# Optimization experiments

Hardware: AMD Instinct MI355X
Metric: run time of the kernel (lower is better)

The kernel has to match this reference:

```python
import jax, jax.numpy as jnp
import numpy as np
import math

G = 8        # groups
ORDER = 2    # Taylor order
GAMMA = 1e-4 # RBF gamma
EPS = 1e-5   # GroupNorm eps


def setup_inputs() -> dict:
    key = jax.random.key(0)
    ks = jax.random.split(key, 6)
    B, C_HI, C_LO, P = 16, 512, 512, 256
    H1 = W1 = 64
    H2 = W2 = 32
    s = 0.02
    return {
        "input_high": jax.random.normal(ks[0], (B, C_HI, H1, W1), jnp.float32),
        "input_low": jax.random.normal(ks[1], (B, C_LO, H2, W2), jnp.float32),
        "Wt": jax.random.normal(ks[2], (P, C_HI), jnp.float32) * s,
        "Wp": jax.random.normal(ks[3], (P, C_LO), jnp.float32) * s,
        "Wg": jax.random.normal(ks[4], (P, C_LO), jnp.float32) * s,
        # grouped 1x1 conv planes -> inplanes1: [G, out_per_group, in_per_group]
        "Wz": jax.random.normal(ks[5], (G, C_HI // G, P // G), jnp.float32) * s,
        "gn_w": jnp.ones((C_HI,), jnp.float32),
        "gn_b": jnp.zeros((C_HI,), jnp.float32),
    }


def _taylor_alpha():
    # alpha_k = sqrt((2*gamma)^k / k! * exp(-2*gamma)) for k = 0..ORDER
    ks = np.arange(ORDER + 1)
    fact = np.array([math.factorial(int(k)) for k in ks], dtype=np.float64)
    a = np.sqrt((2.0 * GAMMA) ** ks / fact * np.exp(-2.0 * GAMMA))
    return jnp.asarray(a, jnp.float32)


def reference(input_high, input_low, Wt, Wp, Wg, Wz, gn_w, gn_b):
    # 1x1-conv projections as channel contractions
    t = jnp.einsum('bchw,oc->bohw', input_high, Wt)   # [b, P, h1, w1]
    p = jnp.einsum('bchw,oc->bohw', input_low, Wp)    # [b, P, h2, w2]
    g = jnp.einsum('bchw,oc->bohw', input_low, Wg)    # [b, P, h2, w2]
    b, c1, h1, w1 = t.shape

    alpha = _taylor_alpha()                            # [ORDER+1]
    # split channels into groups, flatten (c/G)*h*w per group
    tg = t.reshape(b, G, -1)                           # [b, G, N1]
    pg = p.reshape(b, G, -1)                           # [b, G, N2]
    gg = g.reshape(b, G, -1)                           # [b, G, N2]

    # low-rank Taylor feature maps: [b, G, ORDER+1, N]
    t_tay = jnp.stack([tg ** k for k in range(ORDER + 1)], axis=2) * alpha[None, None, :, None]
    p_tay = jnp.stack([pg ** k for k in range(ORDER + 1)], axis=2) * alpha[None, None, :, None]

    att = jnp.einsum('bgkn,bgn->bgk', p_tay, gg)       # [b, G, ORDER+1]
    x = jnp.einsum('bgk,bgkn->bgn', att, t_tay)        # [b, G, N1]
    x = x.reshape(b, G, c1 // G, h1, w1)               # grouped feature map

    # grouped 1x1 conv z: planes -> inplanes1
    z = jnp.einsum('bgihw,goi->bgohw', x, Wz)
    z = z.reshape(b, -1, h1, w1)                       # [b, C_HI, h1, w1]

    # GroupNorm(num_groups=G) with affine, then residual
    zg = z.reshape(b, G, -1)
    mu = zg.mean(axis=-1, keepdims=True)
    var = zg.var(axis=-1, keepdims=True)
    zn = ((zg - mu) * jax.lax.rsqrt(var + EPS)).reshape(z.shape)
    out = zn * gn_w[None, :, None, None] + gn_b[None, :, None, None] + input_high
    return out
```

## Files before the change

### kernel.cpp

```cpp
#include <hip/hip_runtime.h>
#include <math.h>

typedef __attribute__((ext_vector_type(8))) short short8;
typedef __attribute__((ext_vector_type(8))) unsigned short u16x8;
typedef __attribute__((ext_vector_type(4))) float f32x4;

#define EPS_ 1e-5f

__device__ inline unsigned int cvtpk(float a, float b) {
    unsigned int r;
    asm("v_cvt_pk_bf16_f32 %0, %1, %2" : "=v"(r) : "v"(a), "v"(b));
    return r;
}

__device__ inline f32x4 mfma16(u16x8 a, u16x8 b, f32x4 c) {
    return __builtin_amdgcn_mfma_f32_16x16x32_bf16((short8)a, (short8)b, c, 0, 0, 0);
}

__device__ inline void gll16(const unsigned short* g, unsigned short* l) {
    __builtin_amdgcn_global_load_lds(
        (const __attribute__((address_space(1))) unsigned int*)g,
        (__attribute__((address_space(3))) unsigned int*)l, 16, 0, 0);
}

__global__ __launch_bounds__(256)
void k0s(const float* __restrict__ xlo, float* __restrict__ sxsum)
{
    __shared__ float sred[256];
    int blk = blockIdx.x;
    int cgrp = blk & 15, b = blk >> 4;
    int tid = threadIdx.x;
    int cl = tid >> 3, seg = tid & 7;
    int c = cgrp * 32 + cl;
    const float* row = xlo + ((size_t)b * 512 + c) * 1024 + seg * 128;
    float s = 0.f;
#pragma unroll
    for (int i = 0; i < 32; i++) {
        float4 v = ((const float4*)row)[i];
        s += v.x + v.y + v.z + v.w;
    }
    sred[tid] = s;
    __syncthreads();
    if (seg == 0) {
        float t = 0.f;
#pragma unroll
        for (int e = 0; e < 8; e++) t += sred[cl * 8 + e];
        sxsum[(size_t)b * 512 + c] = t;
    }
}

__global__ __launch_bounds__(256)
void k0w_t(const float* __restrict__ Wt, unsigned short* __restrict__ wtb)
{
    int blk = blockIdx.x, tid = threadIdx.x;
    int kc = blk >> 3, sub = blk & 7;
    int idx = sub * 256 + tid;
    int row = idx >> 3, s = idx & 7;
    int colbase = kc * 64 + ((s ^ (row & 7)) << 3);
    const float* sp = Wt + (size_t)row * 512 + colbase;
    float4 v0 = ((const float4*)sp)[0];
    float4 v1 = ((const float4*)sp)[1];
    uint4 q = { cvtpk(v0.x, v0.y), cvtpk(v0.z, v0.w),
                cvtpk(v1.x, v1.y), cvtpk(v1.z, v1.w) };
    *(uint4*)&wtb[(size_t)(kc * 2048 + idx) * 8] = q;
}

#define K1_BODY(C0, VCUR, VNXT, DOPREF)                                          \
  {                                                                              \
    if (DOPREF) {                                                                \
        const float* xc = xlo + ((size_t)b * 512 + (C0) + 64 + cs * 8) * 1024 + hw0 + xrow; \
        _Pragma("unroll")                                                        \
        for (int j = 0; j < 8; j++) VNXT[j] = xc[(size_t)j * 1024];              \
    }                                                                            \
    __syncthreads();                                                             \
    _Pragma("unroll")                                                            \
    for (int k = 0; k < 4; k++) {                                                \
        int idx = k * 256 + tid;                                                 \
        int row = idx >> 3, s = idx & 7;                                         \
        const float* pp = Wp + (size_t)(pbase + row) * 512 + (C0) + s * 8;       \
        const float* pg = Wg + (size_t)(pbase + row) * 512 + (C0) + s * 8;       \
        float4 a0 = ((const float4*)pp)[0], a1 = ((const float4*)pp)[1];         \
        float4 b0 = ((const float4*)pg)[0], b1 = ((const float4*)pg)[1];         \
        uint4 qp = { cvtpk(a0.x,a0.y), cvtpk(a0.z,a0.w),                         \
                     cvtpk(a1.x,a1.y), cvtpk(a1.z,a1.w) };                       \
        uint4 qg = { cvtpk(b0.x,b0.y), cvtpk(b0.z,b0.w),                         \
                     cvtpk(b1.x,b1.y), cvtpk(b1.z,b1.w) };                       \
        int off = row * 64 + ((s ^ (row & 7)) << 3);                             \
        *(uint4*)&sWp[off] = qp;                                                 \
        *(uint4*)&sWg[off] = qg;                                                 \
    }                                                                            \
    {                                                                            \
        uint4 q = { cvtpk(VCUR[0],VCUR[1]), cvtpk(VCUR[2],VCUR[3]),              \
                    cvtpk(VCUR[4],VCUR[5]), cvtpk(VCUR[6],VCUR[7]) };            \
        int phys = cs ^ (xrow & 7);                                              \
        *(uint4*)&sX1[xrow * 64 + phys * 8] = q;                                 \
    }                                                                            \
    __syncthreads();                                                             \
    _Pragma("unroll")                                                            \
    for (int kk = 0; kk < 2; kk++) {                                             \
        u16x8 bf[2];                                                             \
        _Pragma("unroll")                                                        \
        for (int ht = 0; ht < 2; ht++) {                                         \
            int row = ht * 16 + l15;                                             \
            bf[ht] = *(const u16x8*)&sX1[row * 64 + (((kk*4+l4) ^ (row&7)) << 3)]; \
        }                                                                        \
        _Pragma("unroll")                                                        \
        for (int i = 0; i < 2; i++) {                                            \
            int row = w * 32 + i * 16 + l15;                                     \
            int off = row * 64 + (((kk*4+l4) ^ (row&7)) << 3);                   \
            u16x8 ap = *(const u16x8*)&sWp[off];                                 \
            u16x8 ag = *(const u16x8*)&sWg[off];                                 \
            _Pragma("unroll")                                                    \
            for (int ht = 0; ht < 2; ht++) {                                     \
                pacc[i][ht] = mfma16(ap, bf[ht], pacc[i][ht]);                   \
                gacc[i][ht] = mfma16(ag, bf[ht], gacc[i][ht]);                   \
            }                                                                    \
        }                                                                        \
    }                                                                            \
  }

__global__ __launch_bounds__(256, 4)
void k1_att(const float* __restrict__ xlo, const float* __restrict__ Wp,
            const float* __restrict__ Wg, float* __restrict__ att_part)
{
    __shared__ unsigned short sWp[8192];
    __shared__ unsigned short sWg[8192];
    __shared__ unsigned short sX1[2048];

    int tid = threadIdx.x;
    int w = tid >> 6, lane = tid & 63;
    int l15 = lane & 15, l4 = lane >> 4;
    int beta = blockIdx.x;
    int tile = beta & 31, mh = (beta >> 5) & 1, b = beta >> 6;
    int hw0 = tile * 32;
    int pbase = mh * 128;
    int xrow = tid & 31, cs = tid >> 5;

    f32x4 pacc[2][2] = {};
    f32x4 gacc[2][2] = {};

    float vbA[8], vbB[8];
    {
        const float* xc = xlo + ((size_t)b * 512 + cs * 8) * 1024 + hw0 + xrow;
#pragma unroll
        for (int j = 0; j < 8; j++) vbA[j] = xc[(size_t)j * 1024];
    }

    for (int kc2 = 0; kc2 < 4; kc2++) {
        int c0 = kc2 * 128;
        K1_BODY(c0,      vbA, vbB, true);
        K1_BODY(c0 + 64, vbB, vbA, (kc2 < 3));
    }

    float s1 = 0.f, s2 = 0.f;
#pragma unroll
    for (int i = 0; i < 2; i++)
#pragma unroll
        for (int ht = 0; ht < 2; ht++)
#pragma unroll
            for (int r = 0; r < 4; r++) {
                float pv = pacc[i][ht][r], gv = gacc[i][ht][r];
                s1 += pv * gv; s2 += pv * pv * gv;
            }
#pragma unroll
    for (int m = 1; m < 64; m <<= 1) {
        s1 += __shfl_xor(s1, m);
        s2 += __shfl_xor(s2, m);
    }
    if (lane == 0) {
        int g = mh * 4 + w;
        float* dst = att_part + ((size_t)(b * 8 + g) * 32 + tile) * 2;
        dst[0] = s1; dst[1] = s2;
    }
}

__global__ __launch_bounds__(64)
void k1b_coef(const float* __restrict__ Wg, const float* __restrict__ sxsum,
              const float* __restrict__ att_part, float* __restrict__ coef,
              float a0s, float a1s, float a2s)
{
    int bg = blockIdx.x;
    int b = bg >> 3, g = bg & 7;
    int l = threadIdx.x;
    float s0 = 0.f;
    for (int cc = 0; cc < 512; cc += 64) {
        int c = cc + l;
        float cs = 0.f;
#pragma unroll
        for (int pp = 0; pp < 32; pp++) cs += Wg[(size_t)(g * 32 + pp) * 512 + c];
        s0 += cs * sxsum[(size_t)b * 512 + c];
    }
    float s1 = (l < 32) ? att_part[((size_t)bg * 32 + l) * 2 + 0] : 0.f;
    float s2 = (l < 32) ? att_part[((size_t)bg * 32 + l) * 2 + 1] : 0.f;
#pragma unroll
    for (int m = 1; m < 64; m <<= 1) {
        s0 += __shfl_xor(s0, m);
        s1 += __shfl_xor(s1, m);
        s2 += __shfl_xor(s2, m);
    }
    if (l == 0) {
        coef[bg * 3 + 0] = a0s * s0;
        coef[bg * 3 + 1] = a1s * s1;
        coef[bg * 3 + 2] = a2s * s2;
    }
}

#define XLOAD(DST, KC)                                                           \
  { const float* xc = xhi + ((size_t)(b * 512 + (KC) * 64 + w * 8)) * 4096 + hw0 + xrow; \
    _Pragma("unroll")                                                            \
    for (int j = 0; j < 8; j++) DST[j] = xc[(size_t)j * 4096]; }

#define K2CHUNK(KC, WBUF, PBUF, DOPREF, VMC)                                     \
  {                                                                              \
    asm volatile("s_waitcnt lgkmcnt(0)" ::: "memory");                           \
    __builtin_amdgcn_s_barrier();                                                \
    __builtin_amdgcn_sched_barrier(0);                                           \
    {                                 \
        uint4 q = { cvtpk(WBUF[0],WBUF[1]), cvtpk(WBUF[2],WBUF[3]),              \
                    cvtpk(WBUF[4],WBUF[5]), cvtpk(WBUF[6],WBUF[7]) };            \
        int phys = w ^ (xrow & 7);                                               \
        *(uint4*)&sX[xrow * 64 + phys * 8] = q;                                  \
    }                                                                            \
    __builtin_amdgcn_sched_barrier(0);                                           \
    _Pragma("unroll")                                                            \
    for (int k = 0; k < 4; k++) {                                                \
        int u = k * 512 + tid;                                                   \
        gll16(wtb + (((size_t)(KC) * 2048 + u) << 3), &sMain[u << 3]);           \
    }                                                                            \
    __builtin_amdgcn_sched_barrier(0);                                           \
    if (DOPREF) { XLOAD(PBUF, (KC) + 2) }                                        \
    asm volatile("s_waitcnt vmcnt(" #VMC ") lgkmcnt(0)" ::: "memory");           \
    __builtin_amdgcn_s_barrier();                                                \
    __builtin_amdgcn_sched_barrier(0);                                           \
    _Pragma("unroll")                                                            \
    for (int kk = 0; kk < 2; kk++) {                                             \
        u16x8 bf[4];                                                             \
        _Pragma("unroll")                                                        \
        for (int ht = 0; ht < 4; ht++) {                                         \
            int row = ht * 16 + l15;                                             \
            bf[ht] = *(const u16x8*)&sX[row * 64 + (((kk*4+l4) ^ (row&7)) << 3)]; \
        }                                                                        \
        _Pragma("unroll")                                                        \
        for (int i = 0; i < 2; i++) {                                            \
            int row = w * 32 + i * 16 + l15;                                     \
            u16x8 af = *(const u16x8*)&sMain[row * 64 + (((kk*4+l4) ^ (row&7)) << 3)]; \
            _Pragma("unroll")                                                    \
            for (int ht = 0; ht < 4; ht++)                                       \
                acc[i][ht] = mfma16(af, bf[ht], acc[i][ht]);                     \
        }                                                                        \
    }                                                                            \
  }

__global__ __launch_bounds__(512, 4)
void k2_main_g(const float* __restrict__ xhi, const unsigned short* __restrict__ wtb,
               const float* __restrict__ Wz, const float* __restrict__ coef,
               float* __restrict__ zout, float* __restrict__ zstat)
{
    __shared__ unsigned short sMain[16384];
    __shared__ unsigned short sX[4096];

    int tid = threadIdx.x;
    int w = tid >> 6, lane = tid & 63;
    int l15 = lane & 15, l4 = lane >> 4;
    int hwt = blockIdx.x & 63, b = blockIdx.x >> 6;
    int hw0 = hwt * 64;
    int xrow = tid & 63;

    const float* cf = coef + (size_t)(b * 8 + w) * 3;
    float c0v = cf[0], c1v = cf[1], c2v = cf[2];

    f32x4 acc[2][4] = {};

    float vA[8], vB[8], vC[8];
    XLOAD(vA, 0)
    XLOAD(vB, 1)

    K2CHUNK(0, vA, vC, 1, 8)
    K2CHUNK(1, vB, vA, 1, 8)
    K2CHUNK(2, vC, vB, 1, 8)
    K2CHUNK(3, vA, vC, 1, 8)
    K2CHUNK(4, vB, vA, 1, 8)
    K2CHUNK(5, vC, vB, 1, 8)
    K2CHUNK(6, vA, vC, 0, 0)
    K2CHUNK(7, vB, vA, 0, 0)

#pragma unroll
    for (int i = 0; i < 2; i++)
#pragma unroll
        for (int ht = 0; ht < 4; ht++) {
            f32x4 t = acc[i][ht];
            acc[i][ht] = c1v * t + c2v * t * t;
        }
    __syncthreads();

#pragma unroll
    for (int i = 0; i < 2; i++)
#pragma unroll
        for (int ht = 0; ht < 4; ht++) {
            int row = ht * 16 + l15;
            f32x4 xv = acc[i][ht];
            uint2 q = { cvtpk(xv[0], xv[1]), cvtpk(xv[2], xv[3]) };
            int phys = w * 4 + ((i * 2 + (l4 >> 1)) ^ (row & 3));
            *(uint2*)&sMain[row * 256 + phys * 8 + (l4 & 1) * 4] = q;
        }

    float* sR = (float*)sX;
    {
        const float* wr = Wz + (size_t)tid * 32;
        float s = 0.f;
#pragma unroll
        for (int q = 0; q < 8; q++) {
            float4 v = ((const float4*)wr)[q];
            s += v.x + v.y + v.z + v.w;
        }
        sR[tid] = s;
    }
    u16x8 wzf[4];
#pragma unroll
    for (int ot = 0; ot < 4; ot++) {
        const float* wr = Wz + (size_t)(w * 64 + ot * 16 + l15) * 32 + l4 * 8;
        float4 v0 = ((const float4*)wr)[0];
        float4 v1 = ((const float4*)wr)[1];
        uint4 q = { cvtpk(v0.x,v0.y), cvtpk(v0.z,v0.w),
                    cvtpk(v1.x,v1.y), cvtpk(v1.z,v1.w) };
        wzf[ot] = *(u16x8*)&q;
    }
    asm volatile("s_waitcnt lgkmcnt(0)" ::: "memory");
    __builtin_amdgcn_sched_barrier(0);

    float s = 0.f, s2a = 0.f;
    f32x4 zero4 = {0.f, 0.f, 0.f, 0.f};
#pragma unroll
    for (int ht = 0; ht < 4; ht++) {
        int row = ht * 16 + l15;
        u16x8 bfr = *(const u16x8*)&sMain[row * 256 + (w * 4 + (l4 ^ (row & 3))) * 8];
#pragma unroll
        for (int ot = 0; ot < 4; ot++) {
            f32x4 z = mfma16(wzf[ot], bfr, zero4);
            f32x4 rv = *(const f32x4*)&sR[w * 64 + ot * 16 + l4 * 4];
            z = z + c0v * rv;
            float* zp = zout + ((size_t)(b * 512 + w * 64 + ot * 16 + l4 * 4)) * 4096
                      + hw0 + ht * 16 + l15;
#pragma unroll
            for (int r = 0; r < 4; r++) {
                zp[(size_t)r * 4096] = z[r];
                s += z[r]; s2a += z[r] * z[r];
            }
        }
    }
#pragma unroll
    for (int m = 1; m < 64; m <<= 1) {
        s   += __shfl_xor(s, m);
        s2a += __shfl_xor(s2a, m);
    }
    if (lane == 0) {
        atomicAdd(&zstat[(size_t)(b * 8 + w) * 2 + 0], s);
        atomicAdd(&zstat[(size_t)(b * 8 + w) * 2 + 1], s2a);
    }
}

#define K2_BODY(C0, VCUR, VNXT, DOPREF)                                          \
  {                                                                              \
    if (DOPREF) {                                                                \
        const float* xc = xhi + ((size_t)b * 512 + (C0) + 64 + w * 8) * 4096 + hw0 + xrow; \
        _Pragma("unroll")                                                        \
        for (int j = 0; j < 8; j++) VNXT[j] = xc[(size_t)j * 4096];              \
    }                                                                            \
    __syncthreads();                                                             \
    _Pragma("unroll")                                                            \
    for (int k = 0; k < 4; k++) {                                                \
        int idx = k * 512 + tid;                                                 \
        int row = idx >> 3, s = idx & 7;                                         \
        const float* sp = Wt + (size_t)row * 512 + (C0) + s * 8;                 \
        float4 v0 = ((const float4*)sp)[0];                                      \
        float4 v1 = ((const float4*)sp)[1];                                      \
        uint4 q = { cvtpk(v0.x,v0.y), cvtpk(v0.z,v0.w),                          \
                    cvtpk(v1.x,v1.y), cvtpk(v1.z,v1.w) };                        \
        *(uint4*)&sWt[row * 64 + ((s ^ (row & 7)) << 3)] = q;                    \
    }                                                                            \
    {                                                                            \
        uint4 q = { cvtpk(VCUR[0],VCUR[1]), cvtpk(VCUR[2],VCUR[3]),              \
                    cvtpk(VCUR[4],VCUR[5]), cvtpk(VCUR[6],VCUR[7]) };            \
        int phys = w ^ (xrow & 7);                                               \
        *(uint4*)&sX[xrow * 64 + phys * 8] = q;                                  \
    }                                                                            \
    __syncthreads();                                                             \
    _Pragma("unroll")                                                            \
    for (int kk = 0; kk < 2; kk++) {                                             \
        u16x8 bf[4];                                                             \
        _Pragma("unroll")                                                        \
        for (int ht = 0; ht < 4; ht++) {                                         \
            int row = ht * 16 + l15;                                             \
            bf[ht] = *(const u16x8*)&sX[row * 64 + (((kk*4+l4) ^ (row&7)) << 3)]; \
        }                                                                        \
        _Pragma("unroll")                                                        \
        for (int i = 0; i < 2; i++) {                                            \
            int row = w * 32 + i * 16 + l15;                                     \
            u16x8 af = *(const u16x8*)&sWt[row * 64 + (((kk*4+l4) ^ (row&7)) << 3)]; \
            _Pragma("unroll")                                                    \
            for (int ht = 0; ht < 4; ht++)                                       \
                acc[i][ht] = mfma16(af, bf[ht], acc[i][ht]);                     \
        }                                                                        \
    }                                                                            \
  }

__global__ __launch_bounds__(512, 4)
void k2_main_fb(const float* __restrict__ xhi, const float* __restrict__ Wt,
                const float* __restrict__ Wz, const float* __restrict__ coef,
                float* __restrict__ zout, float* __restrict__ zstat)
{
    __shared__ unsigned short sWt[16384];
    __shared__ unsigned short sX[8192];

    int tid = threadIdx.x;
    int w = tid >> 6, lane = tid & 63;
    int l15 = lane & 15, l4 = lane >> 4;
    int hwt = blockIdx.x & 63, b = blockIdx.x >> 6;
    int hw0 = hwt * 64;
    int xrow = tid & 63;

    const float* cf = coef + (size_t)(b * 8 + w) * 3;
    float c0v = cf[0], c1v = cf[1], c2v = cf[2];

    f32x4 acc[2][4] = {};

    float vbA[8], vbB[8];
    {
        const float* xc = xhi + ((size_t)b * 512 + w * 8) * 4096 + hw0 + xrow;
#pragma unroll
        for (int j = 0; j < 8; j++) vbA[j] = xc[(size_t)j * 4096];
    }

    for (int kc2 = 0; kc2 < 4; kc2++) {
        int c0 = kc2 * 128;
        K2_BODY(c0,      vbA, vbB, true);
        K2_BODY(c0 + 64, vbB, vbA, (kc2 < 3));
    }

#pragma unroll
    for (int i = 0; i < 2; i++)
#pragma unroll
        for (int ht = 0; ht < 4; ht++) {
            f32x4 t = acc[i][ht];
            acc[i][ht] = c1v * t + c2v * t * t;
        }
    __syncthreads();
#pragma unroll
    for (int i = 0; i < 2; i++)
#pragma unroll
        for (int ht = 0; ht < 4; ht++) {
            int row = ht * 16 + l15;
            f32x4 xv = acc[i][ht];
            uint2 q = { cvtpk(xv[0], xv[1]), cvtpk(xv[2], xv[3]) };
            int phys = w * 4 + ((i * 2 + (l4 >> 1)) ^ (row & 3));
            *(uint2*)&sWt[row * 256 + phys * 8 + (l4 & 1) * 4] = q;
        }
    float* sR = (float*)sX;
    {
        const float* wr = Wz + (size_t)tid * 32;
        float s = 0.f;
#pragma unroll
        for (int q = 0; q < 8; q++) {
            float4 v = ((const float4*)wr)[q];
            s += v.x + v.y + v.z + v.w;
        }
        sR[tid] = s;
    }
    u16x8 wzf[4];
#pragma unroll
    for (int ot = 0; ot < 4; ot++) {
        const float* wr = Wz + (size_t)(w * 64 + ot * 16 + l15) * 32 + l4 * 8;
        float4 v0 = ((const float4*)wr)[0];
        float4 v1 = ((const float4*)wr)[1];
        uint4 q = { cvtpk(v0.x,v0.y), cvtpk(v0.z,v0.w),
                    cvtpk(v1.x,v1.y), cvtpk(v1.z,v1.w) };
        wzf[ot] = *(u16x8*)&q;
    }
    __syncthreads();

    float s = 0.f, s2a = 0.f;
    f32x4 zero4 = {0.f, 0.f, 0.f, 0.f};
#pragma unroll
    for (int ht = 0; ht < 4; ht++) {
        int row = ht * 16 + l15;
        u16x8 bfr = *(const u16x8*)&sWt[row * 256 + (w * 4 + (l4 ^ (row & 3))) * 8];
#pragma unroll
        for (int ot = 0; ot < 4; ot++) {
            f32x4 z = mfma16(wzf[ot], bfr, zero4);
            f32x4 rv = *(const f32x4*)&sR[w * 64 + ot * 16 + l4 * 4];
            z = z + c0v * rv;
            float* zp = zout + ((size_t)(b * 512 + w * 64 + ot * 16 + l4 * 4)) * 4096
                      + hw0 + ht * 16 + l15;
#pragma unroll
            for (int r = 0; r < 4; r++) {
                zp[(size_t)r * 4096] = z[r];
                s += z[r]; s2a += z[r] * z[r];
            }
        }
    }
#pragma unroll
    for (int m = 1; m < 64; m <<= 1) {
        s   += __shfl_xor(s, m);
        s2a += __shfl_xor(s2a, m);
    }
    if (lane == 0) {
        atomicAdd(&zstat[(size_t)(b * 8 + w) * 2 + 0], s);
        atomicAdd(&zstat[(size_t)(b * 8 + w) * 2 + 1], s2a);
    }
}

__global__ void k2b_gn(const float* __restrict__ zstat, float* __restrict__ gnstat)
{
    int t = threadIdx.x;
    if (t >= 128) return;
    float S = zstat[t * 2], S2 = zstat[t * 2 + 1];
    const float N = 64.0f * 4096.0f;
    float mean = S / N;
    float var = S2 / N - mean * mean;
    var = var < 0.f ? 0.f : var;
    gnstat[t * 2] = mean;
    gnstat[t * 2 + 1] = rsqrtf(var + EPS_);
}

__global__ __launch_bounds__(256)
void k3_final(float* __restrict__ out, const float* __restrict__ xhi,
              const float* __restrict__ gnstat, const float* __restrict__ gnw,
              const float* __restrict__ gnb)
{
#pragma unroll
    for (int k = 0; k < 4; k++) {
        size_t idx = (size_t)blockIdx.x * 1024 + (size_t)k * 256 + threadIdx.x;
        size_t e = idx * 4;
        int ch = (int)((e >> 12) & 511);
        int b  = (int)(e >> 21);
        int gg = ch >> 6;
        const float* gs = gnstat + (size_t)(b * 8 + gg) * 2;
        float mean = gs[0];
        float w = gnw[ch] * gs[1];
        float bb = gnb[ch];
        float4 z = ((const float4*)out)[idx];
        float4 xv = ((const float4*)xhi)[idx];
        float4 r;
        r.x = (z.x - mean) * w + bb + xv.x;
        r.y = (z.y - mean) * w + bb + xv.y;
        r.z = (z.z - mean) * w + bb + xv.z;
        r.w = (z.w - mean) * w + bb + xv.w;
        ((float4*)out)[idx] = r;
    }
}

extern "C" void kernel_launch(void* const* d_in, const int* in_sizes, int n_in,
                              void* d_out, int out_size, void* d_ws, size_t ws_size,
                              hipStream_t stream) {
    (void)in_sizes; (void)n_in; (void)out_size;
    const float* xhi = (const float*)d_in[0];
    const float* xlo = (const float*)d_in[1];
    const float* Wt  = (const float*)d_in[2];
    const float* Wp  = (const float*)d_in[3];
    const float* Wg  = (const float*)d_in[4];
    const float* Wz  = (const float*)d_in[5];
    const float* gnw = (const float*)d_in[6];
    const float* gnb = (const float*)d_in[7];
    float* out = (float*)d_out;
    float* ws  = (float*)d_ws;

    float* sxsum    = ws;
    float* att_part = ws + 8192;
    float* coef     = ws + 16384;
    float* zstat    = ws + 16768;
    float* gnstat   = ws + 17024;
    unsigned short* wtb = (unsigned short*)((char*)d_ws + 69632);

    const size_t WS_NEED = 69632 + 262144;
    bool use_gll = (ws_size >= WS_NEED);

    double g2 = 2.0e-4;
    double ee = exp(-g2);
    float a0s = (float)ee;
    float a1s = (float)(g2 * ee);
    float a2s = (float)(g2 * g2 * 0.5 * ee);

    k0s     <<<dim3(256),  dim3(256), 0, stream>>>(xlo, sxsum);
    k1_att  <<<dim3(1024), dim3(256), 0, stream>>>(xlo, Wp, Wg, att_part);
    k1b_coef<<<dim3(128),  dim3(64),  0, stream>>>(Wg, sxsum, att_part, coef, a0s, a1s, a2s);
    hipMemsetAsync(zstat, 0, 256 * sizeof(float), stream);
    if (use_gll) {
        k0w_t    <<<dim3(64),   dim3(256), 0, stream>>>(Wt, wtb);
        k2_main_g<<<dim3(1024), dim3(512), 0, stream>>>(xhi, wtb, Wz, coef, out, zstat);
    } else {
        k2_main_fb<<<dim3(1024), dim3(512), 0, stream>>>(xhi, Wt, Wz, coef, out, zstat);
    }
    k2b_gn  <<<dim3(1),    dim3(128), 0, stream>>>(zstat, gnstat);
    k3_final<<<dim3(8192), dim3(256), 0, stream>>>(out, xhi, gnstat, gnw, gnb);
}
```

Measured before the change: 211.3 us.

## Widen main GEMM tile to 128 spatial positions to halve Wt reloads

Each block of the fused projection kernel now covers 128 spatial positions instead of 64, halving the grid. Each Wt chunk staged into shared memory is therefore reused across twice as many columns, which cuts global/L2 traffic for the weight. The x prefetch changes from triple to double buffering with 16 values per thread. The grouped Wz epilogue is split into two passes because the wider tile's bf16 activations no longer fit in one shared buffer. Host launches are reordered so the memset and weight conversion run earlier; the cost is more registers per thread, extra barriers and a smaller grid.

```diff
diff --git a/kernel.cpp b/kernel.cpp
--- a/kernel.cpp
+++ b/kernel.cpp
@@ -205,20 +205,21 @@
     }
 }
 
-#define XLOAD(DST, KC)                                                           \
-  { const float* xc = xhi + ((size_t)(b * 512 + (KC) * 64 + w * 8)) * 4096 + hw0 + xrow; \
-    _Pragma("unroll")                                                            \
-    for (int j = 0; j < 8; j++) DST[j] = xc[(size_t)j * 4096]; }
-
-#define K2CHUNK(KC, WBUF, PBUF, DOPREF, VMC)                                     \
+#define XLOADW(DST, KC)                                                          \
+  { const float* xc = xhi + ((size_t)(b * 512 + (KC) * 64 + cq * 16)) * 4096 + hw0 + xrow; \
+    _Pragma("unroll")                                                            \
+    for (int j = 0; j < 16; j++) DST[j] = xc[(size_t)j * 4096]; }
+
+#define K2WCHUNK(KC, WBUF, PBUF, DOPREF, VMC)                                    \
   {                                                                              \
     asm volatile("s_waitcnt lgkmcnt(0)" ::: "memory");                           \
     __builtin_amdgcn_s_barrier();                                                \
     __builtin_amdgcn_sched_barrier(0);                                           \
-    {                                 \
-        uint4 q = { cvtpk(WBUF[0],WBUF[1]), cvtpk(WBUF[2],WBUF[3]),              \
-                    cvtpk(WBUF[4],WBUF[5]), cvtpk(WBUF[6],WBUF[7]) };            \
-        int phys = w ^ (xrow & 7);                                               \
+    _Pragma("unroll")                                                            \
+    for (int h = 0; h < 2; h++) {     \
+        uint4 q = { cvtpk(WBUF[h*8+0],WBUF[h*8+1]), cvtpk(WBUF[h*8+2],WBUF[h*8+3]), \
+                    cvtpk(WBUF[h*8+4],WBUF[h*8+5]), cvtpk(WBUF[h*8+6],WBUF[h*8+7]) }; \
+        int phys = (cq * 2 + h) ^ (xrow & 7);                                    \
         *(uint4*)&sX[xrow * 64 + phys * 8] = q;                                  \
     }                                                                            \
     __builtin_amdgcn_sched_barrier(0);                                           \
@@ -228,15 +229,15 @@
         gll16(wtb + (((size_t)(KC) * 2048 + u) << 3), &sMain[u << 3]);           \
     }                                                                            \
     __builtin_amdgcn_sched_barrier(0);                                           \
-    if (DOPREF) { XLOAD(PBUF, (KC) + 2) }                                        \
+    if (DOPREF) { XLOADW(PBUF, (KC) + 1) }                                       \
     asm volatile("s_waitcnt vmcnt(" #VMC ") lgkmcnt(0)" ::: "memory");           \
     __builtin_amdgcn_s_barrier();                                                \
     __builtin_amdgcn_sched_barrier(0);                                           \
     _Pragma("unroll")                                                            \
     for (int kk = 0; kk < 2; kk++) {                                             \
-        u16x8 bf[4];                                                             \
-        _Pragma("unroll")                                                        \
-        for (int ht = 0; ht < 4; ht++) {                                         \
+        u16x8 bf[8];                                                             \
+        _Pragma("unroll")                                                        \
+        for (int ht = 0; ht < 8; ht++) {                                         \
             int row = ht * 16 + l15;                                             \
             bf[ht] = *(const u16x8*)&sX[row * 64 + (((kk*4+l4) ^ (row&7)) << 3)]; \
         }                                                                        \
@@ -245,7 +246,7 @@
             int row = w * 32 + i * 16 + l15;                                     \
             u16x8 af = *(const u16x8*)&sMain[row * 64 + (((kk*4+l4) ^ (row&7)) << 3)]; \
             _Pragma("unroll")                                                    \
-            for (int ht = 0; ht < 4; ht++)                                       \
+            for (int ht = 0; ht < 8; ht++)                                       \
                 acc[i][ht] = mfma16(af, bf[ht], acc[i][ht]);                     \
         }                                                                        \
     }                                                                            \
@@ -257,52 +258,40 @@
                float* __restrict__ zout, float* __restrict__ zstat)
 {
     __shared__ unsigned short sMain[16384];
-    __shared__ unsigned short sX[4096];
+    __shared__ unsigned short sX[8192];
 
     int tid = threadIdx.x;
     int w = tid >> 6, lane = tid & 63;
     int l15 = lane & 15, l4 = lane >> 4;
-    int hwt = blockIdx.x & 63, b = blockIdx.x >> 6;
-    int hw0 = hwt * 64;
-    int xrow = tid & 63;
+    int hwt = blockIdx.x & 31, b = blockIdx.x >> 5;
+    int hw0 = hwt * 128;
+    int xrow = tid & 127, cq = tid >> 7;
 
     const float* cf = coef + (size_t)(b * 8 + w) * 3;
-    float c0v = cf[0], c1v = cf[1], c2v = cf[2];
-
-    f32x4 acc[2][4] = {};
-
-    float vA[8], vB[8], vC[8];
-    XLOAD(vA, 0)
-    XLOAD(vB, 1)
-
-    K2CHUNK(0, vA, vC, 1, 8)
-    K2CHUNK(1, vB, vA, 1, 8)
-    K2CHUNK(2, vC, vB, 1, 8)
-    K2CHUNK(3, vA, vC, 1, 8)
-    K2CHUNK(4, vB, vA, 1, 8)
-    K2CHUNK(5, vC, vB, 1, 8)
-    K2CHUNK(6, vA, vC, 0, 0)
-    K2CHUNK(7, vB, vA, 0, 0)
+    float c1v = cf[1], c2v = cf[2];
+
+    f32x4 acc[2][8] = {};
+
+    float vA[16], vB[16];
+    XLOADW(vA, 0)
+
+    K2WCHUNK(0, vA, vB, 1, 16)
+    K2WCHUNK(1, vB, vA, 1, 16)
+    K2WCHUNK(2, vA, vB, 1, 16)
+    K2WCHUNK(3, vB, vA, 1, 16)
+    K2WCHUNK(4, vA, vB, 1, 16)
+    K2WCHUNK(5, vB, vA, 1, 16)
+    K2WCHUNK(6, vA, vB, 1, 16)
+    K2WCHUNK(7, vB, vA, 0, 0)
 
 #pragma unroll
     for (int i = 0; i < 2; i++)
 #pragma unroll
-        for (int ht = 0; ht < 4; ht++) {
+        for (int ht = 0; ht < 8; ht++) {
             f32x4 t = acc[i][ht];
             acc[i][ht] = c1v * t + c2v * t * t;
         }
     __syncthreads();
-
-#pragma unroll
-    for (int i = 0; i < 2; i++)
-#pragma unroll
-        for (int ht = 0; ht < 4; ht++) {
-            int row = ht * 16 + l15;
-            f32x4 xv = acc[i][ht];
-            uint2 q = { cvtpk(xv[0], xv[1]), cvtpk(xv[2], xv[3]) };
-            int phys = w * 4 + ((i * 2 + (l4 >> 1)) ^ (row & 3));
-            *(uint2*)&sMain[row * 256 + phys * 8 + (l4 & 1) * 4] = q;
-        }
 
     float* sR = (float*)sX;
     {
@@ -315,47 +304,64 @@
         }
         sR[tid] = s;
     }
-    u16x8 wzf[4];
-#pragma unroll
-    for (int ot = 0; ot < 4; ot++) {
-        const float* wr = Wz + (size_t)(w * 64 + ot * 16 + l15) * 32 + l4 * 8;
-        float4 v0 = ((const float4*)wr)[0];
-        float4 v1 = ((const float4*)wr)[1];
-        uint4 q = { cvtpk(v0.x,v0.y), cvtpk(v0.z,v0.w),
-                    cvtpk(v1.x,v1.y), cvtpk(v1.z,v1.w) };
-        wzf[ot] = *(u16x8*)&q;
-    }
-    asm volatile("s_waitcnt lgkmcnt(0)" ::: "memory");
-    __builtin_amdgcn_sched_barrier(0);
-
-    float s = 0.f, s2a = 0.f;
+
     f32x4 zero4 = {0.f, 0.f, 0.f, 0.f};
 #pragma unroll
-    for (int ht = 0; ht < 4; ht++) {
-        int row = ht * 16 + l15;
-        u16x8 bfr = *(const u16x8*)&sMain[row * 256 + (w * 4 + (l4 ^ (row & 3))) * 8];
+    for (int pass = 0; pass < 2; pass++) {
+        if ((w >> 2) == pass) {
+#pragma unroll
+            for (int i = 0; i < 2; i++)
+#pragma unroll
+                for (int ht = 0; ht < 8; ht++) {
+                    int row = ht * 16 + l15;
+                    f32x4 xv = acc[i][ht];
+                    uint2 q = { cvtpk(xv[0], xv[1]), cvtpk(xv[2], xv[3]) };
+                    int phys = (w & 3) * 4 + ((i * 2 + (l4 >> 1)) ^ (row & 3));
+                    *(uint2*)&sMain[row * 128 + phys * 8 + (l4 & 1) * 4] = q;
+                }
+        }
+        __syncthreads();
+        int g = pass * 4 + (w >> 1);
+        float c0p = coef[(size_t)(b * 8 + g) * 3];
+        u16x8 wzf[4];
 #pragma unroll
         for (int ot = 0; ot < 4; ot++) {
-            f32x4 z = mfma16(wzf[ot], bfr, zero4);
-            f32x4 rv = *(const f32x4*)&sR[w * 64 + ot * 16 + l4 * 4];
-            z = z + c0v * rv;
-            float* zp = zout + ((size_t)(b * 512 + w * 64 + ot * 16 + l4 * 4)) * 4096
-                      + hw0 + ht * 16 + l15;
-#pragma unroll
-            for (int r = 0; r < 4; r++) {
-                zp[(size_t)r * 4096] = z[r];
-                s += z[r]; s2a += z[r] * z[r];
+            const float* wr = Wz + (size_t)(g * 64 + ot * 16 + l15) * 32 + l4 * 8;
+            float4 v0 = ((const float4*)wr)[0];
+            float4 v1 = ((const float4*)wr)[1];
+            uint4 q = { cvtpk(v0.x,v0.y), cvtpk(v0.z,v0.w),
+                        cvtpk(v1.x,v1.y), cvtpk(v1.z,v1.w) };
+            wzf[ot] = *(u16x8*)&q;
+        }
+        float s = 0.f, s2a = 0.f;
+#pragma unroll
+        for (int ht = 0; ht < 4; ht++) {
+            int row = (w & 1) * 64 + ht * 16 + l15;
+            u16x8 bfr = *(const u16x8*)&sMain[row * 128 + ((g & 3) * 4 + (l4 ^ (row & 3))) * 8];
+#pragma unroll
+            for (int ot = 0; ot < 4; ot++) {
+                f32x4 z = mfma16(wzf[ot], bfr, zero4);
+                f32x4 rv = *(const f32x4*)&sR[g * 64 + ot * 16 + l4 * 4];
+                z = z + c0p * rv;
+                float* zp = zout + ((size_t)(b * 512 + g * 64 + ot * 16 + l4 * 4)) * 4096
+                          + hw0 + row;
+#pragma unroll
+                for (int r = 0; r < 4; r++) {
+                    zp[(size_t)r * 4096] = z[r];
+                    s += z[r]; s2a += z[r] * z[r];
+                }
             }
         }
-    }
-#pragma unroll
-    for (int m = 1; m < 64; m <<= 1) {
-        s   += __shfl_xor(s, m);
-        s2a += __shfl_xor(s2a, m);
-    }
-    if (lane == 0) {
-        atomicAdd(&zstat[(size_t)(b * 8 + w) * 2 + 0], s);
-        atomicAdd(&zstat[(size_t)(b * 8 + w) * 2 + 1], s2a);
+#pragma unroll
+        for (int m = 1; m < 64; m <<= 1) {
+            s   += __shfl_xor(s, m);
+            s2a += __shfl_xor(s2a, m);
+        }
+        if (lane == 0) {
+            atomicAdd(&zstat[(size_t)(b * 8 + g) * 2 + 0], s);
+            atomicAdd(&zstat[(size_t)(b * 8 + g) * 2 + 1], s2a);
+        }
+        __syncthreads();
     }
 }
 
@@ -580,13 +586,14 @@
     float a1s = (float)(g2 * ee);
     float a2s = (float)(g2 * g2 * 0.5 * ee);
 
+    hipMemsetAsync(zstat, 0, 256 * sizeof(float), stream);
     k0s     <<<dim3(256),  dim3(256), 0, stream>>>(xlo, sxsum);
+    if (use_gll)
+        k0w_t <<<dim3(64),   dim3(256), 0, stream>>>(Wt, wtb);
     k1_att  <<<dim3(1024), dim3(256), 0, stream>>>(xlo, Wp, Wg, att_part);
     k1b_coef<<<dim3(128),  dim3(64),  0, stream>>>(Wg, sxsum, att_part, coef, a0s, a1s, a2s);
-    hipMemsetAsync(zstat, 0, 256 * sizeof(float), stream);
     if (use_gll) {
-        k0w_t    <<<dim3(64),   dim3(256), 0, stream>>>(Wt, wtb);
-        k2_main_g<<<dim3(1024), dim3(512), 0, stream>>>(xhi, wtb, Wz, coef, out, zstat);
+        k2_main_g<<<dim3(512),  dim3(512), 0, stream>>>(xhi, wtb, Wz, coef, out, zstat);
     } else {
         k2_main_fb<<<dim3(1024), dim3(512), 0, stream>>>(xhi, Wt, Wz, coef, out, zstat);
     }
```

Measured after the change: 224.2 us. 6.1% more time.
